# Kernel optimization log

Hardware: AMD Instinct MI355X
Metric: run time of the kernel (lower is better)

## Reference

```python
import jax, jax.numpy as jnp
import numpy as np

B, S, E, R = 64, 2048, 256, 50


def setup_inputs() -> dict:
    key = jax.random.key(0)
    ks = jax.random.split(key, 22)
    n = lambda k, shp, s=0.05: (jax.random.normal(k, shp, jnp.float32) * s)
    d = {
        "encoder_o": jax.random.normal(ks[0], (B, S, E), jnp.float32),
        "h0": jax.random.normal(ks[1], (1, B, E), jnp.float32),
        "c0": jax.random.normal(ks[2], (1, B, E), jnp.float32),
        "r_in": jax.random.randint(ks[3], (B,), 0, R),
        "k1": jax.random.randint(ks[4], (B, 1), 0, S),
        "k2": jax.random.randint(ks[5], (B, 1), 0, S),
        "W_ih": n(ks[6], (4 * E, E)),
        "W_hh": n(ks[7], (4 * E, E)),
        "b_ih": n(ks[8], (4 * E,)),
        "b_hh": n(ks[9], (4 * E,)),
        "W_attn": n(ks[10], (E, 2 * E)),
        "b_attn": n(ks[11], (E,)),
        "W_conv": n(ks[12], (E, 2 * E, 3)),
        "b_conv": n(ks[13], (E,)),
        "sos_emb": n(ks[14], (1, E)),
        "rel_emb": n(ks[15], (R, E)),
        "W_rel": n(ks[16], (R, E)),
        "b_rel": n(ks[17], (R,)),
        "W_ent1": n(ks[18], (1, E)),
        "b_ent1": n(ks[19], (1,)),
        "W_ent2": n(ks[20], (1, E)),
        "b_ent2": n(ks[21], (1,)),
    }
    return d


def reference(encoder_o, h0, c0, r_in, k1, k2, W_ih, W_hh, b_ih, b_hh,
              W_attn, b_attn, W_conv, b_conv, sos_emb, rel_emb,
              W_rel, b_rel, W_ent1, b_ent1, W_ent2, b_ent2):
    Bx, Sx, Ex = encoder_o.shape

    def lstm_step(x, h, c):  # single decode step, x/h/c: [B,E]
        gates = x @ W_ih.T + h @ W_hh.T + (b_ih + b_hh)  # [B,4E]
        i, f, g, o = jnp.split(gates, 4, axis=-1)        # PyTorch gate order i,f,g,o
        c2 = jax.nn.sigmoid(f) * c + jax.nn.sigmoid(i) * jnp.tanh(g)
        h2 = jax.nn.sigmoid(o) * jnp.tanh(c2)
        return h2, c2

    def attend(q):  # Luong dot attention + tanh(linear(cat(mix,q))); q: [B,E]
        scores = jnp.einsum('be,bse->bs', q, encoder_o)
        attn = jax.nn.softmax(scores, axis=-1)
        mix = jnp.einsum('bs,bse->be', attn, encoder_o)
        comb = jnp.concatenate([mix, q], axis=-1)        # [B,2E]
        return jnp.tanh(comb @ W_attn.T + b_attn)

    def step(x, h, c):
        h2, c2 = lstm_step(x, h, c)
        return attend(h2), h2, c2

    kern = jnp.transpose(W_conv, (2, 1, 0))  # [3, 2E, E] for NWC/WIO

    def ent_heads(o):  # o: [B,E]
        vec = jnp.broadcast_to(o[:, None, :], (Bx, Sx, Ex))  # seq_and_vec
        feat = jnp.concatenate([encoder_o, vec], axis=-1)    # [B,S,2E]
        conv = jax.lax.conv_general_dilated(
            feat, kern, (1,), 'SAME',
            dimension_numbers=('NWC', 'WIO', 'NWC')) + b_conv
        conv = jax.nn.relu(conv)                             # [B,S,E]
        e1 = conv @ W_ent1.T + b_ent1                        # [B,S,1]
        e2 = conv @ W_ent2.T + b_ent2
        return e1, e2

    h, c = h0[0], c0[0]
    # t1: <sos> -> relation logits
    x = jnp.broadcast_to(sos_emb[0], (Bx, Ex))
    out1, h, c = step(x, h, c)
    t1_out = out1 @ W_rel.T + b_rel                          # [B,R]
    # t2: relation embedding -> entity-1 span heads
    out2, h, c = step(rel_emb[r_in], h, c)
    e1a, e2a = ent_heads(out2)
    # t3: gathered k1+k2 encoder vectors -> entity-2 span heads
    idx = jnp.arange(Bx)
    kk = encoder_o[idx, k1[:, 0]] + encoder_o[idx, k2[:, 0]]  # vectorized seq_gather
    out3, h, c = step(kk, h, c)
    e1b, e2b = ent_heads(out3)
    # pack outputs: [B, R + 4*S]
    return jnp.concatenate(
        [t1_out, e1a[..., 0], e2a[..., 0], e1b[..., 0], e2b[..., 0]], axis=1)
```

## Files before the change

kernel.cpp:

```cpp
#include <hip/hip_runtime.h>
#include <hip/hip_bf16.h>

#define EE 256
#define SS 2048
#define BB 64
#define RN 50
#define OSTR 8242
#define NCH 32

typedef __attribute__((ext_vector_type(4))) float vf4;
typedef __attribute__((ext_vector_type(8))) short s8v;
typedef __attribute__((ext_vector_type(4))) short s4v;
typedef __attribute__((ext_vector_type(4))) unsigned short u16x4;
typedef __attribute__((ext_vector_type(2))) unsigned int u32x2;
typedef __attribute__((ext_vector_type(4))) unsigned int u32x4;

__device__ __forceinline__ unsigned short f2bf(float f){
  __hip_bfloat16 h = __float2bfloat16(f);
  return *reinterpret_cast<unsigned short*>(&h);
}
__device__ __forceinline__ unsigned int f2bf2(float a, float b){
  __hip_bfloat162 h = __float22bfloat162_rn(make_float2(a, b));
  return *reinterpret_cast<unsigned int*>(&h);
}
__device__ __forceinline__ float sigm(float x){ return 1.0f/(1.0f + __expf(-x)); }
__device__ __forceinline__ float dot4(vf4 a, vf4 b){ return a.x*b.x + a.y*b.y + a.z*b.z + a.w*b.w; }

__device__ __forceinline__ vf4 mfma16(s4v a, s4v b, vf4 c){
#if __has_builtin(__builtin_amdgcn_mfma_f32_16x16x16bf16_1k)
  return __builtin_amdgcn_mfma_f32_16x16x16bf16_1k(a, b, c, 0, 0, 0);
#else
  vf4 d;
  asm volatile("v_mfma_f32_16x16x16_bf16 %0, %1, %2, %3\n\ts_nop 7\n\ts_nop 7"
               : "=v"(d) : "v"(a), "v"(b), "v"(c));
  return d;
#endif
}

__device__ __forceinline__ void gload_lds16(const void* g, void* l){
  __builtin_amdgcn_global_load_lds(
      (const __attribute__((address_space(1))) unsigned int*)g,
      (__attribute__((address_space(3))) unsigned int*)l, 16, 0, 0);
}

__global__ __launch_bounds__(256) void k_prep(
  const float* __restrict__ enc, const float* __restrict__ h0, const float* __restrict__ c0,
  const int* __restrict__ r_in, const int* __restrict__ k1, const int* __restrict__ k2,
  const float* __restrict__ sos, const float* __restrict__ rel,
  const float* __restrict__ W_conv,
  float* __restrict__ xT, float* __restrict__ hT0, float* __restrict__ cT,
  unsigned short* __restrict__ WT, unsigned short* __restrict__ Bp)
{
  int bid = blockIdx.x, t = threadIdx.x;
  if (bid < 256){
    int part = bid >> 6, b = bid & 63;
    if (part == 0){
      xT[(size_t)0*EE*BB + t*BB + b] = sos[t];
    } else if (part == 1){
      xT[(size_t)1*EE*BB + t*BB + b] = rel[r_in[b]*EE + t];
    } else if (part == 2){
      int i1 = k1[b], i2 = k2[b];
      xT[(size_t)2*EE*BB + t*BB + b] =
        enc[((size_t)b*SS + i1)*EE + t] + enc[((size_t)b*SS + i2)*EE + t];
    } else {
      hT0[t*BB + b] = h0[b*EE + t];
      cT [t*BB + b] = c0[b*EE + t];
    }
  } else if (bid < 512){
    int o = bid - 256;
    for (int r = t; r < 768; r += 256)
      WT[(size_t)r*EE + o] = f2bf(W_conv[(size_t)o*1536 + 768 + r]);
  } else {
    int gid = (bid - 512)*256 + t;
    int kc  = gid >> 10;
    int rem = gid & 1023;
    int ni  = rem >> 6;
    int l   = rem & 63;
    int o   = ni*16 + (l & 15);
    int kbase = kc*32 + ((l >> 4) << 3);
    u16x4 lo4, hi4;
    #pragma unroll
    for (int j=0;j<8;++j){
      int k = kbase + j; int ktap = k >> 8; int i = k & 255;
      unsigned short v = f2bf(W_conv[((size_t)o*512 + i)*3 + ktap]);
      if (j<4){ if(j==0)lo4.x=v; else if(j==1)lo4.y=v; else if(j==2)lo4.z=v; else lo4.w=v; }
      else    { if(j==4)hi4.x=v; else if(j==5)hi4.y=v; else if(j==6)hi4.z=v; else hi4.w=v; }
    }
    u16x4* dst = (u16x4*)(Bp + (size_t)gid*8);
    dst[0] = lo4; dst[1] = hi4;
  }
}

__global__ __launch_bounds__(1024) void k_step(
  const float* __restrict__ hT_cur, const float* __restrict__ xT_st,
  const float* __restrict__ W_ih, const float* __restrict__ W_hh,
  const float* __restrict__ b_ih, const float* __restrict__ b_hh,
  float* __restrict__ cT, float* __restrict__ hT_next, float* __restrict__ hs_st)
{
  int e = blockIdx.x, tid = threadIdx.x;
  int w = tid >> 6, b = tid & 63;
  int g = w & 3, kq = w >> 2;
  int grow = g*EE + e;
  const float* wh = W_hh + (size_t)grow*EE + kq*64;
  const float* wi = W_ih + (size_t)grow*EE + kq*64;
  const float* hT = hT_cur + kq*64*BB;
  const float* xv = xT_st + kq*64*BB;
  float acc = (kq == 0) ? (b_ih[grow] + b_hh[grow]) : 0.0f;
  #pragma unroll 4
  for (int k4 = 0; k4 < 16; ++k4){
    vf4 wh4 = *(const vf4*)(wh + k4*4);
    vf4 wi4 = *(const vf4*)(wi + k4*4);
    int k = k4*4;
    acc += hT[(k+0)*BB+b]*wh4.x + hT[(k+1)*BB+b]*wh4.y
         + hT[(k+2)*BB+b]*wh4.z + hT[(k+3)*BB+b]*wh4.w;
    acc += xv[(k+0)*BB+b]*wi4.x + xv[(k+1)*BB+b]*wi4.y
         + xv[(k+2)*BB+b]*wi4.z + xv[(k+3)*BB+b]*wi4.w;
  }
  __shared__ float sm[16][BB];
  sm[w][b] = acc;
  __syncthreads();
  if (tid < BB){
    float iv = sm[0][tid]+sm[4][tid]+sm[8][tid] +sm[12][tid];
    float fv = sm[1][tid]+sm[5][tid]+sm[9][tid] +sm[13][tid];
    float gv = sm[2][tid]+sm[6][tid]+sm[10][tid]+sm[14][tid];
    float ov = sm[3][tid]+sm[7][tid]+sm[11][tid]+sm[15][tid];
    float cprev = cT[e*BB + tid];
    float cn = sigm(fv)*cprev + sigm(iv)*tanhf(gv);
    float hn = sigm(ov)*tanhf(cn);
    cT[e*BB + tid] = cn;
    hT_next[e*BB + tid] = hn;
    hs_st[(size_t)tid*EE + e] = hn;
  }
}

__global__ __launch_bounds__(256) void k_attend(
  const float* __restrict__ enc, const float* __restrict__ hs,
  float* __restrict__ mixc, float* __restrict__ stats,
  unsigned short* __restrict__ encb)
{
  int bid = blockIdx.x; int b = bid >> 5, ch = bid & 31;
  int tid = threadIdx.x, lane = tid & 63, wv = tid >> 6;
  int rs = lane >> 4, cg = lane & 15;
  __shared__ float qsm[3][EE];
  __shared__ float sc[3][64];
  __shared__ vf4 mpart[4][3][64];

  const float* chunk = enc + ((size_t)b*SS + ch*64)*EE;

  vf4 dat[4][4];
  #pragma unroll
  for (int i=0;i<4;++i){
    const vf4* rp = (const vf4*)(chunk + (size_t)(wv*16 + i*4 + rs)*EE + cg*16);
    #pragma unroll
    for (int v=0;v<4;++v) dat[i][v] = rp[v];
  }
  for (int i = tid; i < 3*EE; i += 256)
    qsm[i>>8][i&255] = hs[((size_t)(i>>8)*BB + b)*EE + (i&255)];
  __syncthreads();

  {
    vf4 q0[4], q1[4], q2[4];
    #pragma unroll
    for (int v=0;v<4;++v){
      q0[v] = *(const vf4*)(qsm[0] + cg*16 + v*4);
      q1[v] = *(const vf4*)(qsm[1] + cg*16 + v*4);
      q2[v] = *(const vf4*)(qsm[2] + cg*16 + v*4);
    }
    #pragma unroll
    for (int i=0;i<4;++i){
      float a0=0.f, a1=0.f, a2=0.f;
      #pragma unroll
      for (int v=0;v<4;++v){
        a0 += dot4(dat[i][v], q0[v]);
        a1 += dot4(dat[i][v], q1[v]);
        a2 += dot4(dat[i][v], q2[v]);
      }
      #pragma unroll
      for (int d=1; d<16; d<<=1){
        a0 += __shfl_xor(a0,d); a1 += __shfl_xor(a1,d); a2 += __shfl_xor(a2,d);
      }
      if (cg == 0){
        int r = wv*16 + i*4 + rs;
        sc[0][r]=a0; sc[1][r]=a1; sc[2][r]=a2;
      }
    }
  }
  __syncthreads();

  float e0, e1, e2;
  {
    float s0 = sc[0][lane], s1 = sc[1][lane], s2 = sc[2][lane];
    float m0=s0, m1=s1, m2=s2;
    #pragma unroll
    for (int d=1; d<64; d<<=1){
      m0 = fmaxf(m0, __shfl_xor(m0,d));
      m1 = fmaxf(m1, __shfl_xor(m1,d));
      m2 = fmaxf(m2, __shfl_xor(m2,d));
    }
    e0 = __expf(s0-m0); e1 = __expf(s1-m1); e2 = __expf(s2-m2);
    float l0=e0, l1=e1, l2=e2;
    #pragma unroll
    for (int d=1; d<64; d<<=1){
      l0 += __shfl_xor(l0,d); l1 += __shfl_xor(l1,d); l2 += __shfl_xor(l2,d);
    }
    if (tid == 0){
      int o0 = ((0*BB+b)*NCH + ch)*2; stats[o0]=m0; stats[o0+1]=l0;
      int o1 = ((1*BB+b)*NCH + ch)*2; stats[o1]=m1; stats[o1+1]=l1;
      int o2 = ((2*BB+b)*NCH + ch)*2; stats[o2]=m2; stats[o2+1]=l2;
    }
  }

  vf4 A0[4], A1[4], A2[4];
  #pragma unroll
  for (int v=0;v<4;++v){ A0[v]=(vf4)0.0f; A1[v]=(vf4)0.0f; A2[v]=(vf4)0.0f; }
  #pragma unroll
  for (int i=0;i<4;++i){
    int r = wv*16 + i*4 + rs;
    int gs = ch*64 + r;
    float w0 = __shfl(e0, r), w1 = __shfl(e1, r), w2 = __shfl(e2, r);
    if (encb){
      int key = ((gs + 1) & 7) << 4;
      char* base = (char*)encb + ((size_t)b*SS + gs)*512;
      u32x4 lo4, hi4;
      lo4.x = f2bf2(dat[i][0].x, dat[i][0].y); lo4.y = f2bf2(dat[i][0].z, dat[i][0].w);
      lo4.z = f2bf2(dat[i][1].x, dat[i][1].y); lo4.w = f2bf2(dat[i][1].z, dat[i][1].w);
      hi4.x = f2bf2(dat[i][2].x, dat[i][2].y); hi4.y = f2bf2(dat[i][2].z, dat[i][2].w);
      hi4.z = f2bf2(dat[i][3].x, dat[i][3].y); hi4.w = f2bf2(dat[i][3].z, dat[i][3].w);
      *(u32x4*)(base + ((cg*32     ) ^ key)) = lo4;
      *(u32x4*)(base + ((cg*32 + 16) ^ key)) = hi4;
    }
    #pragma unroll
    for (int v=0;v<4;++v){
      A0[v] += dat[i][v]*w0; A1[v] += dat[i][v]*w1; A2[v] += dat[i][v]*w2;
    }
  }
  #pragma unroll
  for (int v=0;v<4;++v){
    #pragma unroll
    for (int d=16; d<64; d<<=1){
      A0[v].x += __shfl_xor(A0[v].x,d); A0[v].y += __shfl_xor(A0[v].y,d);
      A0[v].z += __shfl_xor(A0[v].z,d); A0[v].w += __shfl_xor(A0[v].w,d);
      A1[v].x += __shfl_xor(A1[v].x,d); A1[v].y += __shfl_xor(A1[v].y,d);
      A1[v].z += __shfl_xor(A1[v].z,d); A1[v].w += __shfl_xor(A1[v].w,d);
      A2[v].x += __shfl_xor(A2[v].x,d); A2[v].y += __shfl_xor(A2[v].y,d);
      A2[v].z += __shfl_xor(A2[v].z,d); A2[v].w += __shfl_xor(A2[v].w,d);
    }
  }
  if (rs == 0){
    #pragma unroll
    for (int v=0;v<4;++v){
      mpart[wv][0][cg*4+v] = A0[v];
      mpart[wv][1][cg*4+v] = A1[v];
      mpart[wv][2][cg*4+v] = A2[v];
    }
  }
  __syncthreads();
  if (tid < 192){
    int q = tid >> 6, e4 = tid & 63;
    vf4 sum = mpart[0][q][e4] + mpart[1][q][e4] + mpart[2][q][e4] + mpart[3][q][e4];
    *(vf4*)(mixc + ((size_t)(q*BB+b)*NCH + ch)*EE + e4*4) = sum;
  }
}

__global__ __launch_bounds__(256) void k_post(
  const float* __restrict__ mixc, const float* __restrict__ hs,
  const float* __restrict__ stats,
  const float* __restrict__ W_attn, const float* __restrict__ b_attn,
  const float* __restrict__ W_rel, const float* __restrict__ b_rel,
  const unsigned short* __restrict__ WT, const float* __restrict__ b_conv,
  float* __restrict__ out, float* __restrict__ vv)
{
  int b = blockIdx.x, t = threadIdx.x;
  __shared__ float comb[3][2*EE];
  __shared__ float o1[EE], o2s[EE], o3s[EE];
  #pragma unroll
  for (int q=0;q<3;q++){
    float M = -1e30f;
    for (int c=0;c<NCH;c++) M = fmaxf(M, stats[((q*BB+b)*NCH + c)*2]);
    float L = 0.f, macc = 0.f;
    for (int c=0;c<NCH;c++){
      int o = ((q*BB+b)*NCH + c)*2;
      float e = __expf(stats[o]-M);
      L += stats[o+1]*e;
      macc += mixc[((size_t)(q*BB+b)*NCH + c)*EE + t] * e;
    }
    comb[q][t] = macc / L;
    comb[q][EE+t] = hs[((size_t)q*BB + b)*EE + t];
  }
  __syncthreads();
  float a0 = b_attn[t], a1 = a0, a2 = a0;
  const vf4* wr = (const vf4*)(W_attn + (size_t)t*2*EE);
  const vf4* c0v = (const vf4*)comb[0];
  const vf4* c1v = (const vf4*)comb[1];
  const vf4* c2v = (const vf4*)comb[2];
  #pragma unroll 4
  for (int k=0;k<2*EE/4;++k){
    vf4 w = wr[k];
    a0 += dot4(w, c0v[k]); a1 += dot4(w, c1v[k]); a2 += dot4(w, c2v[k]);
  }
  o1[t]=tanhf(a0); o2s[t]=tanhf(a1); o3s[t]=tanhf(a2);
  __syncthreads();
  if (t < RN){
    float acc = b_rel[t];
    const vf4* wrel = (const vf4*)(W_rel + (size_t)t*EE);
    const vf4* ov = (const vf4*)o1;
    for (int k=0;k<EE/4;++k) acc += dot4(wrel[k], ov[k]);
    out[(size_t)b*OSTR + t] = acc;
  }
  float va0=0,va1=0,va2=0, vb0=0,vb1=0,vb2=0;
  for (int i=0;i<EE;++i){
    float x2 = o2s[i], x3 = o3s[i];
    const unsigned short* wt = WT + (size_t)i*3*EE + t;
    float w0 = __uint_as_float(((unsigned int)wt[0]) << 16);
    float w1 = __uint_as_float(((unsigned int)wt[EE]) << 16);
    float w2 = __uint_as_float(((unsigned int)wt[2*EE]) << 16);
    va0 += x2*w0; va1 += x2*w1; va2 += x2*w2;
    vb0 += x3*w0; vb1 += x3*w1; vb2 += x3*w2;
  }
  float bc = b_conv[t];
  vv[((0*3+0)*BB + b)*EE + t] = va0+va1+va2+bc;
  vv[((0*3+1)*BB + b)*EE + t] = va1+va2+bc;
  vv[((0*3+2)*BB + b)*EE + t] = va0+va1+bc;
  vv[((1*3+0)*BB + b)*EE + t] = vb0+vb1+vb2+bc;
  vv[((1*3+1)*BB + b)*EE + t] = vb1+vb2+bc;
  vv[((1*3+2)*BB + b)*EE + t] = vb0+vb1+bc;
}

__global__ __launch_bounds__(256, 3) void k_conv(
  const float* __restrict__ enc, const unsigned short* __restrict__ encb,
  const unsigned short* __restrict__ Bp,
  const float* __restrict__ vv,
  const float* __restrict__ W_e1, const float* __restrict__ b_e1,
  const float* __restrict__ W_e2, const float* __restrict__ b_e2,
  float* __restrict__ out)
{
  int stile = blockIdx.x, b = blockIdx.y;
  int s0 = stile*64;
  int tid = threadIdx.x, lane = tid & 63, w = tid >> 6;
  int lo = lane & 15, hi = lane >> 4;
  __shared__ __align__(16) unsigned short Ab[66*256];
  __shared__ float part2[4][64][4];

  if (encb){
    const char* ebase = (const char*)encb + (size_t)b*SS*512;
    for (int base = 0; base < 66*32; base += 256){
      int idx = base + tid;
      if (idx < 66*32){
        int r = idx >> 5, c = idx & 31;
        int srow = s0 - 1 + r;
        srow = srow < 0 ? 0 : (srow > SS-1 ? SS-1 : srow);
        gload_lds16(ebase + (size_t)srow*512 + c*16, (char*)Ab + idx*16);
      }
    }
    __syncthreads();
    if (stile == 0 || stile == 31){
      if (stile == 0  && tid < 32) *(vf4*)((char*)Ab + tid*16) = (vf4)0.0f;
      if (stile == 31 && tid < 32) *(vf4*)((char*)Ab + 65*512 + tid*16) = (vf4)0.0f;
      __syncthreads();
    }
  } else {
    const float* eb = enc + (size_t)b*SS*EE;
    for (int idx = tid; idx < 66*64; idx += 256){
      int r = idx >> 6, c4 = idx & 63;
      int s = s0 - 1 + r;
      vf4 v = (vf4)0.0f;
      if (s >= 0 && s < SS) v = *(const vf4*)(eb + (size_t)s*EE + c4*4);
      u32x2 pk; pk.x = f2bf2(v.x, v.y); pk.y = f2bf2(v.z, v.w);
      int byte = (r*512 + c4*8) ^ ((r & 7) << 4);
      *(u32x2*)((char*)Ab + byte) = pk;
    }
    __syncthreads();
  }

  vf4 acc[4][4];
  #pragma unroll
  for (int oi=0;oi<4;++oi){
    #pragma unroll
    for (int si=0;si<4;++si) acc[oi][si] = (vf4)0.0f;
  }
  const s8v* Bp8 = (const s8v*)Bp;
  s8v bf[4], bfn[4];
  #pragma unroll
  for (int oi=0;oi<4;++oi) bf[oi] = Bp8[((0*16 + (w*4+oi)) << 6) + lane];

  for (int kc=0; kc<24; ++kc){
    int ktap = kc >> 3;
    int colb = ((kc & 7) << 6) + (hi << 4);
    s8v af[4];
    #pragma unroll
    for (int si=0;si<4;++si){
      int row = si*16 + lo + ktap;
      int byte = row*512 + (colb ^ ((row & 7) << 4));
      af[si] = *(const s8v*)((const char*)Ab + byte);
    }
    if (kc < 23){
      #pragma unroll
      for (int oi=0;oi<4;++oi) bfn[oi] = Bp8[(((kc+1)*16 + (w*4+oi)) << 6) + lane];
    }
    #pragma unroll
    for (int oi=0;oi<4;++oi){
      #pragma unroll
      for (int si=0;si<4;++si)
        acc[oi][si] = __builtin_amdgcn_mfma_f32_16x16x32_bf16(bf[oi], af[si], acc[oi][si], 0, 0, 0);
    }
    #pragma unroll
    for (int oi=0;oi<4;++oi) bf[oi] = bfn[oi];
  }

  bool firstTile = (s0 == 0), lastTile = (s0 + 64 == SS);
  vf4 vaI[4], vbI[4]; s4v aw[4];
  #pragma unroll
  for (int oi=0;oi<4;++oi){
    int o4 = w*64 + oi*16 + hi*4;
    vaI[oi] = *(const vf4*)(vv + ((0*3+0)*BB + b)*EE + o4);
    vbI[oi] = *(const vf4*)(vv + ((1*3+0)*BB + b)*EE + o4);
    vf4 w1 = *(const vf4*)(W_e1 + o4);
    vf4 w2 = *(const vf4*)(W_e2 + o4);
    float e0 = (lo==0) ? w1.x : ((lo==1) ? w2.x : 0.0f);
    float e1 = (lo==0) ? w1.y : ((lo==1) ? w2.y : 0.0f);
    float e2 = (lo==0) ? w1.z : ((lo==1) ? w2.z : 0.0f);
    float e3 = (lo==0) ? w1.w : ((lo==1) ? w2.w : 0.0f);
    u32x2 t; t.x = f2bf2(e0, e1); t.y = f2bf2(e2, e3);
    aw[oi] = __builtin_bit_cast(s4v, t);
  }
  #pragma unroll
  for (int si=0; si<4; ++si){
    vf4 Da = (vf4)0.0f, Db = (vf4)0.0f;
    #pragma unroll
    for (int oi=0; oi<4; ++oi){
      int o4 = w*64 + oi*16 + hi*4;
      vf4 c = acc[oi][si];
      vf4 va = vaI[oi], vb = vbI[oi];
      if (firstTile && si==0 && lo==0){
        va = *(const vf4*)(vv + ((0*3+1)*BB + b)*EE + o4);
        vb = *(const vf4*)(vv + ((1*3+1)*BB + b)*EE + o4);
      }
      if (lastTile && si==3 && lo==15){
        va = *(const vf4*)(vv + ((0*3+2)*BB + b)*EE + o4);
        vb = *(const vf4*)(vv + ((1*3+2)*BB + b)*EE + o4);
      }
      float a0 = fmaxf(c.x+va.x,0.f), a1 = fmaxf(c.y+va.y,0.f);
      float a2 = fmaxf(c.z+va.z,0.f), a3 = fmaxf(c.w+va.w,0.f);
      float b0 = fmaxf(c.x+vb.x,0.f), b1 = fmaxf(c.y+vb.y,0.f);
      float b2 = fmaxf(c.z+vb.z,0.f), b3 = fmaxf(c.w+vb.w,0.f);
      u32x2 ta; ta.x = f2bf2(a0,a1); ta.y = f2bf2(a2,a3);
      u32x2 tb; tb.x = f2bf2(b0,b1); tb.y = f2bf2(b2,b3);
      Da = mfma16(aw[oi], __builtin_bit_cast(s4v, ta), Da);
      Db = mfma16(aw[oi], __builtin_bit_cast(s4v, tb), Db);
    }
    if (hi == 0){
      vf4 pk; pk.x = Da.x; pk.y = Da.y; pk.z = Db.x; pk.w = Db.y;
      *(vf4*)&part2[w][si*16+lo][0] = pk;
    }
  }
  __syncthreads();
  {
    int s = tid >> 2, c = tid & 3;
    float r = part2[0][s][c] + part2[1][s][c] + part2[2][s][c] + part2[3][s][c];
    r += (c & 1) ? b_e2[0] : b_e1[0];
    out[(size_t)b*OSTR + RN + c*SS + (s0 + s)] = r;
  }
}

extern "C" void kernel_launch(void* const* d_in, const int* in_sizes, int n_in,
                              void* d_out, int out_size, void* d_ws, size_t ws_size,
                              hipStream_t stream)
{
  const float* enc   = (const float*)d_in[0];
  const float* h0    = (const float*)d_in[1];
  const float* c0    = (const float*)d_in[2];
  const int*   r_in  = (const int*)d_in[3];
  const int*   k1    = (const int*)d_in[4];
  const int*   k2    = (const int*)d_in[5];
  const float* W_ih  = (const float*)d_in[6];
  const float* W_hh  = (const float*)d_in[7];
  const float* b_ih  = (const float*)d_in[8];
  const float* b_hh  = (const float*)d_in[9];
  const float* W_attn= (const float*)d_in[10];
  const float* b_attn= (const float*)d_in[11];
  const float* W_conv= (const float*)d_in[12];
  const float* b_conv= (const float*)d_in[13];
  const float* sos   = (const float*)d_in[14];
  const float* rel   = (const float*)d_in[15];
  const float* W_rel = (const float*)d_in[16];
  const float* b_rel = (const float*)d_in[17];
  const float* W_e1  = (const float*)d_in[18];
  const float* b_e1  = (const float*)d_in[19];
  const float* W_e2  = (const float*)d_in[20];
  const float* b_e2  = (const float*)d_in[21];
  float* out = (float*)d_out;
  char* ws = (char*)d_ws;

  float* hs    = (float*)(ws);
  float* vv    = (float*)(ws + 196608);
  float* stats = (float*)(ws + 589824);
  float* mixc  = (float*)(ws + 638976);
  unsigned short* Bp = (unsigned short*)(ws + 6930432);
  float* xT    = (float*)(ws + 7323648);
  float* hTa   = (float*)(ws + 7520256);
  float* hTb   = (float*)(ws + 7585792);
  float* cT    = (float*)(ws + 7651328);
  unsigned short* WT = (unsigned short*)(ws + 7716864);
  size_t encb_off = 8110080;
  size_t need = encb_off + (size_t)BB*SS*EE*2;
  unsigned short* encb = (ws_size >= need) ? (unsigned short*)(ws + encb_off) : nullptr;

  hipLaunchKernelGGL(k_prep,  dim3(608), dim3(256), 0, stream,
                     enc,h0,c0,r_in,k1,k2,sos,rel,W_conv, xT,hTa,cT, WT,Bp);
  hipLaunchKernelGGL(k_step,  dim3(256), dim3(1024), 0, stream,
                     hTa, xT + 0*EE*BB, W_ih,W_hh,b_ih,b_hh, cT, hTb, hs + 0*BB*EE);
  hipLaunchKernelGGL(k_step,  dim3(256), dim3(1024), 0, stream,
                     hTb, xT + 1*EE*BB, W_ih,W_hh,b_ih,b_hh, cT, hTa, hs + 1*BB*EE);
  hipLaunchKernelGGL(k_step,  dim3(256), dim3(1024), 0, stream,
                     hTa, xT + 2*EE*BB, W_ih,W_hh,b_ih,b_hh, cT, hTb, hs + 2*BB*EE);
  hipLaunchKernelGGL(k_attend,dim3(2048), dim3(256), 0, stream, enc, hs, mixc, stats, encb);
  hipLaunchKernelGGL(k_post,  dim3(64),  dim3(256), 0, stream,
                     mixc, hs, stats, W_attn,b_attn, W_rel,b_rel, WT, b_conv, out, vv);
  hipLaunchKernelGGL(k_conv,  dim3(32,64), dim3(256), 0, stream,
                     enc, encb, Bp, vv, W_e1,b_e1, W_e2,b_e2, out);
}
```

Measured before the change: 182.9 us.

## Restructure attention kernel to 128-row chunks with two-pass encoder reads

The attention kernel now handles 128 sequence rows per block instead of 64, halving the grid and the number of chunk partials that k_post has to merge. It no longer keeps the encoder tile in registers. The score pass streams rows directly from global memory, the exp weights are kept in shared memory, and a second pass rereads each row with one float4 per lane to do the weighted sum and the bf16 encoder copy. This removes register pressure and the cross-lane shuffle reduction for the mix vector. The cost is reading the encoder chunk twice, where the second read may or may not hit in cache.

After: 188.9 us. 1.03x slower.

```diff
diff --git a/kernel.cpp b/kernel.cpp
--- a/kernel.cpp
+++ b/kernel.cpp
@@ -6,14 +6,13 @@
 #define BB 64
 #define RN 50
 #define OSTR 8242
-#define NCH 32
+#define NCH 16
 
 typedef __attribute__((ext_vector_type(4))) float vf4;
 typedef __attribute__((ext_vector_type(8))) short s8v;
 typedef __attribute__((ext_vector_type(4))) short s4v;
 typedef __attribute__((ext_vector_type(4))) unsigned short u16x4;
 typedef __attribute__((ext_vector_type(2))) unsigned int u32x2;
-typedef __attribute__((ext_vector_type(4))) unsigned int u32x4;
 
 __device__ __forceinline__ unsigned short f2bf(float f){
   __hip_bfloat16 h = __float2bfloat16(f);
@@ -138,67 +137,59 @@
   float* __restrict__ mixc, float* __restrict__ stats,
   unsigned short* __restrict__ encb)
 {
-  int bid = blockIdx.x; int b = bid >> 5, ch = bid & 31;
+  int bid = blockIdx.x; int b = bid >> 4, ch = bid & 15;
   int tid = threadIdx.x, lane = tid & 63, wv = tid >> 6;
-  int rs = lane >> 4, cg = lane & 15;
-  __shared__ float qsm[3][EE];
-  __shared__ float sc[3][64];
+  __shared__ float sc[3][128];
   __shared__ vf4 mpart[4][3][64];
 
-  const float* chunk = enc + ((size_t)b*SS + ch*64)*EE;
-
-  vf4 dat[4][4];
-  #pragma unroll
-  for (int i=0;i<4;++i){
-    const vf4* rp = (const vf4*)(chunk + (size_t)(wv*16 + i*4 + rs)*EE + cg*16);
-    #pragma unroll
-    for (int v=0;v<4;++v) dat[i][v] = rp[v];
-  }
-  for (int i = tid; i < 3*EE; i += 256)
-    qsm[i>>8][i&255] = hs[((size_t)(i>>8)*BB + b)*EE + (i&255)];
-  __syncthreads();
+  const float* chunk = enc + ((size_t)b*SS + ch*128)*EE;
 
   {
+    int rs = lane >> 4, cg = lane & 15;
     vf4 q0[4], q1[4], q2[4];
     #pragma unroll
-    for (int v=0;v<4;++v){
-      q0[v] = *(const vf4*)(qsm[0] + cg*16 + v*4);
-      q1[v] = *(const vf4*)(qsm[1] + cg*16 + v*4);
-      q2[v] = *(const vf4*)(qsm[2] + cg*16 + v*4);
-    }
-    #pragma unroll
-    for (int i=0;i<4;++i){
+    for (int v=0; v<4; ++v){
+      q0[v] = *(const vf4*)(hs + ((size_t)0*BB + b)*EE + cg*16 + v*4);
+      q1[v] = *(const vf4*)(hs + ((size_t)1*BB + b)*EE + cg*16 + v*4);
+      q2[v] = *(const vf4*)(hs + ((size_t)2*BB + b)*EE + cg*16 + v*4);
+    }
+    #pragma unroll
+    for (int i=0; i<8; ++i){
+      int r = wv*32 + i*4 + rs;
+      const vf4* rp = (const vf4*)(chunk + (size_t)r*EE + cg*16);
       float a0=0.f, a1=0.f, a2=0.f;
       #pragma unroll
-      for (int v=0;v<4;++v){
-        a0 += dot4(dat[i][v], q0[v]);
-        a1 += dot4(dat[i][v], q1[v]);
-        a2 += dot4(dat[i][v], q2[v]);
+      for (int v=0; v<4; ++v){
+        vf4 ev = rp[v];
+        a0 += dot4(ev, q0[v]); a1 += dot4(ev, q1[v]); a2 += dot4(ev, q2[v]);
       }
       #pragma unroll
       for (int d=1; d<16; d<<=1){
         a0 += __shfl_xor(a0,d); a1 += __shfl_xor(a1,d); a2 += __shfl_xor(a2,d);
       }
-      if (cg == 0){
-        int r = wv*16 + i*4 + rs;
-        sc[0][r]=a0; sc[1][r]=a1; sc[2][r]=a2;
-      }
-    }
-  }
-  __syncthreads();
-
-  float e0, e1, e2;
-  {
-    float s0 = sc[0][lane], s1 = sc[1][lane], s2 = sc[2][lane];
-    float m0=s0, m1=s1, m2=s2;
+      if (cg == 0){ sc[0][r]=a0; sc[1][r]=a1; sc[2][r]=a2; }
+    }
+  }
+  __syncthreads();
+
+  if (tid < 64){
+    float s0a = sc[0][tid], s0b = sc[0][64+tid];
+    float s1a = sc[1][tid], s1b = sc[1][64+tid];
+    float s2a = sc[2][tid], s2b = sc[2][64+tid];
+    float m0 = fmaxf(s0a,s0b), m1 = fmaxf(s1a,s1b), m2 = fmaxf(s2a,s2b);
     #pragma unroll
     for (int d=1; d<64; d<<=1){
       m0 = fmaxf(m0, __shfl_xor(m0,d));
       m1 = fmaxf(m1, __shfl_xor(m1,d));
       m2 = fmaxf(m2, __shfl_xor(m2,d));
     }
-    e0 = __expf(s0-m0); e1 = __expf(s1-m1); e2 = __expf(s2-m2);
-    float l0=e0, l1=e1, l2=e2;
+    float e0a = __expf(s0a-m0), e0b = __expf(s0b-m0);
+    float e1a = __expf(s1a-m1), e1b = __expf(s1b-m1);
+    float e2a = __expf(s2a-m2), e2b = __expf(s2b-m2);
+    sc[0][tid]=e0a; sc[0][64+tid]=e0b;
+    sc[1][tid]=e1a; sc[1][64+tid]=e1b;
+    sc[2][tid]=e2a; sc[2][64+tid]=e2b;
+    float l0=e0a+e0b, l1=e1a+e1b, l2=e2a+e2b;
     #pragma unroll
     for (int d=1; d<64; d<<=1){
       l0 += __shfl_xor(l0,d); l1 += __shfl_xor(l1,d); l2 += __shfl_xor(l2,d);
@@ -209,50 +200,24 @@
       int o2 = ((2*BB+b)*NCH + ch)*2; stats[o2]=m2; stats[o2+1]=l2;
     }
   }
-
-  vf4 A0[4], A1[4], A2[4];
-  #pragma unroll
-  for (int v=0;v<4;++v){ A0[v]=(vf4)0.0f; A1[v]=(vf4)0.0f; A2[v]=(vf4)0.0f; }
-  #pragma unroll
-  for (int i=0;i<4;++i){
-    int r = wv*16 + i*4 + rs;
-    int gs = ch*64 + r;
-    float w0 = __shfl(e0, r), w1 = __shfl(e1, r), w2 = __shfl(e2, r);
-    if (encb){
-      int key = ((gs + 1) & 7) << 4;
-      char* base = (char*)encb + ((size_t)b*SS + gs)*512;
-      u32x4 lo4, hi4;
-      lo4.x = f2bf2(dat[i][0].x, dat[i][0].y); lo4.y = f2bf2(dat[i][0].z, dat[i][0].w);
-      lo4.z = f2bf2(dat[i][1].x, dat[i][1].y); lo4.w = f2bf2(dat[i][1].z, dat[i][1].w);
-      hi4.x = f2bf2(dat[i][2].x, dat[i][2].y); hi4.y = f2bf2(dat[i][2].z, dat[i][2].w);
-      hi4.z = f2bf2(dat[i][3].x, dat[i][3].y); hi4.w = f2bf2(dat[i][3].z, dat[i][3].w);
-      *(u32x4*)(base + ((cg*32     ) ^ key)) = lo4;
-      *(u32x4*)(base + ((cg*32 + 16) ^ key)) = hi4;
-    }
-    #pragma unroll
-    for (int v=0;v<4;++v){
-      A0[v] += dat[i][v]*w0; A1[v] += dat[i][v]*w1; A2[v] += dat[i][v]*w2;
-    }
-  }
-  #pragma unroll
-  for (int v=0;v<4;++v){
-    #pragma unroll
-    for (int d=16; d<64; d<<=1){
-      A0[v].x += __shfl_xor(A0[v].x,d); A0[v].y += __shfl_xor(A0[v].y,d);
-      A0[v].z += __shfl_xor(A0[v].z,d); A0[v].w += __shfl_xor(A0[v].w,d);
-      A1[v].x += __shfl_xor(A1[v].x,d); A1[v].y += __shfl_xor(A1[v].y,d);
-      A1[v].z += __shfl_xor(A1[v].z,d); A1[v].w += __shfl_xor(A1[v].w,d);
-      A2[v].x += __shfl_xor(A2[v].x,d); A2[v].y += __shfl_xor(A2[v].y,d);
-      A2[v].z += __shfl_xor(A2[v].z,d); A2[v].w += __shfl_xor(A2[v].w,d);
-    }
-  }
-  if (rs == 0){
-    #pragma unroll
-    for (int v=0;v<4;++v){
-      mpart[wv][0][cg*4+v] = A0[v];
-      mpart[wv][1][cg*4+v] = A1[v];
-      mpart[wv][2][cg*4+v] = A2[v];
-    }
+  __syncthreads();
+
+  {
+    vf4 A0 = (vf4)0.0f, A1 = (vf4)0.0f, A2 = (vf4)0.0f;
+    #pragma unroll 4
+    for (int j=0;j<32;++j){
+      int r = wv*32 + j;
+      int gs = ch*128 + r;
+      vf4 ev = *(const vf4*)(chunk + (size_t)r*EE + lane*4);
+      if (encb){
+        u32x2 pk; pk.x = f2bf2(ev.x, ev.y); pk.y = f2bf2(ev.z, ev.w);
+        int key = ((gs + 1) & 7) << 4;
+        *(u32x2*)((char*)encb + ((size_t)b*SS + gs)*512 + ((lane*8) ^ key)) = pk;
+      }
+      float w0 = sc[0][r], w1 = sc[1][r], w2 = sc[2][r];
+      A0 += ev*w0; A1 += ev*w1; A2 += ev*w2;
+    }
+    mpart[wv][0][lane]=A0; mpart[wv][1][lane]=A1; mpart[wv][2][lane]=A2;
   }
   __syncthreads();
   if (tid < 192){
@@ -513,7 +478,7 @@
                      hTb, xT + 1*EE*BB, W_ih,W_hh,b_ih,b_hh, cT, hTa, hs + 1*BB*EE);
   hipLaunchKernelGGL(k_step,  dim3(256), dim3(1024), 0, stream,
                      hTa, xT + 2*EE*BB, W_ih,W_hh,b_ih,b_hh, cT, hTb, hs + 2*BB*EE);
-  hipLaunchKernelGGL(k_attend,dim3(2048), dim3(256), 0, stream, enc, hs, mixc, stats, encb);
+  hipLaunchKernelGGL(k_attend,dim3(1024), dim3(256), 0, stream, enc, hs, mixc, stats, encb);
   hipLaunchKernelGGL(k_post,  dim3(64),  dim3(256), 0, stream,
                      mixc, hs, stats, W_attn,b_attn, W_rel,b_rel, WT, b_conv, out, vv);
   hipLaunchKernelGGL(k_conv,  dim3(32,64), dim3(256), 0, stream,
```
